# Kernel tuning notes

Hardware: AMD Instinct MI355X
Metric: run time of the kernel (lower is better)

Reference implementation:

```python
import jax, jax.numpy as jnp
import numpy as np
from jax import lax

L = 15      # time_conv_size
STRIDE = 2


def setup_inputs() -> dict:
    key = jax.random.key(0)
    k1, k2, k3 = jax.random.split(key, 3)
    x = jax.random.normal(k1, (8, 4096, 64), dtype=jnp.float32)
    w1 = jax.random.normal(k2, (L,), dtype=jnp.float32)
    w2 = jax.random.normal(k3, (L,), dtype=jnp.float32)
    return {"x": x, "w1": w1, "w2": w2}


def reference(x, w1, w2):
    # x: [B, T, C]; w1, w2: [L]
    B, T, C = x.shape
    p = L // 2
    # --- weighted local mean: mu[b,t,c] = sum_k w1[k] * x_pad[b,t+k,c] ---
    x_pad = jnp.pad(x, ((0, 0), (p, p), (0, 0)))
    mu = sum(w1[k] * x_pad[:, k:k + T, :] for k in range(L))  # [B,T,C]
    # --- centered diagonal bilinear (covariance) pooling ---
    xc_pad = jnp.pad(x - mu, ((0, 0), (p, p), (0, 0)))  # [B, T+2p, C]
    # strided window indices: I = ceil(T/STRIDE) windows of length L
    starts = jnp.arange(0, T, STRIDE)                   # [I]
    idx = starts[:, None] + jnp.arange(L)[None, :]      # [I, L]
    win = xc_pad[:, idx, :]                             # [B, I, L, C]
    sigma = jnp.einsum('bilc,l,bild->bicd', win, w2, win)
    I = starts.shape[0]
    sigma = sigma.reshape(B, I, C * C)
    mu_s = mu[:, ::STRIDE, :]                           # [B, I, C]
    out = jnp.concatenate([mu_s, sigma], axis=-1)       # [B, I, C + C*C]
    # K.l2_normalize over last axis (epsilon=1e-12)
    denom = lax.rsqrt(jnp.maximum(jnp.sum(out * out, axis=-1, keepdims=True), 1e-12))
    return out * denom
```

## Files before the change

kernel.cpp:

```cpp
#include <hip/hip_runtime.h>

#define Tdim 4096
#define Bdim 8
#define Cdim 64
#define Ldim 15
#define Idim 2048
#define OUTW 4160
#define G    4
#define RX   (2*G + 27)
#define RXC  (2*G + 13)

typedef float v4f __attribute__((ext_vector_type(4)));

__global__ __launch_bounds__(256, 6) void cbp_kernel(const float* __restrict__ x,
                                                     const float* __restrict__ w1,
                                                     const float* __restrict__ w2,
                                                     float* __restrict__ out) {
    __shared__ float xbuf[RX][64];
    __shared__ float xcs[RXC][64];
    __shared__ float mus[G][64];
    __shared__ float red[G][4];

    const int tid = threadIdx.x;
    const int blk = blockIdx.x;
    const int b  = blk >> 9;
    const int i0 = (blk & 511) << 2;
    const int s0 = i0 << 1;

    const float* xb = x + (size_t)b * (Tdim * Cdim);
    for (int v = tid; v < RX * 16; v += 256) {
        const int r  = v >> 4;
        const int c4 = (v & 15) << 2;
        const int t  = s0 - 14 + r;
        float4 val = make_float4(0.f, 0.f, 0.f, 0.f);
        if (t >= 0 && t < Tdim) val = *(const float4*)(xb + (size_t)t * Cdim + c4);
        *(float4*)(&xbuf[r][c4]) = val;
    }
    __syncthreads();

    for (int v = tid; v < RXC * 16; v += 256) {
        const int j  = v >> 4;
        const int c4 = (v & 15) << 2;
        const int t  = s0 - 7 + j;
        float4 m = make_float4(0.f, 0.f, 0.f, 0.f);
#pragma unroll
        for (int k = 0; k < Ldim; ++k) {
            const float w = w1[k];
            const float4 xv = *(const float4*)(&xbuf[j + k][c4]);
            m.x = fmaf(w, xv.x, m.x);
            m.y = fmaf(w, xv.y, m.y);
            m.z = fmaf(w, xv.z, m.z);
            m.w = fmaf(w, xv.w, m.w);
        }
        const float4 xv = *(const float4*)(&xbuf[j + 7][c4]);
        float4 xc = make_float4(0.f, 0.f, 0.f, 0.f);
        if (t >= 0 && t < Tdim)
            xc = make_float4(xv.x - m.x, xv.y - m.y, xv.z - m.z, xv.w - m.w);
        *(float4*)(&xcs[j][c4]) = xc;
        if (j >= 7 && j <= 13 && ((j - 7) & 1) == 0)
            *(float4*)(&mus[(j - 7) >> 1][c4]) = m;
    }
    __syncthreads();

    const int c0 = (tid >> 4) << 2;
    const int d0 = (tid & 15) << 2;

#pragma unroll
    for (int g = 0; g < G; ++g) {
        float acc[4][4];
#pragma unroll
        for (int cc = 0; cc < 4; ++cc)
#pragma unroll
            for (int dd = 0; dd < 4; ++dd) acc[cc][dd] = 0.f;

#pragma unroll
        for (int l = 0; l < Ldim; ++l) {
            const int r = 2 * g + l;
            const float4 xd = *(const float4*)(&xcs[r][d0]);
            const float4 xc = *(const float4*)(&xcs[r][c0]);
            const float w  = w2[l];
            const float a0 = w * xc.x, a1 = w * xc.y, a2 = w * xc.z, a3 = w * xc.w;
            acc[0][0] = fmaf(a0, xd.x, acc[0][0]);
            acc[0][1] = fmaf(a0, xd.y, acc[0][1]);
            acc[0][2] = fmaf(a0, xd.z, acc[0][2]);
            acc[0][3] = fmaf(a0, xd.w, acc[0][3]);
            acc[1][0] = fmaf(a1, xd.x, acc[1][0]);
            acc[1][1] = fmaf(a1, xd.y, acc[1][1]);
            acc[1][2] = fmaf(a1, xd.z, acc[1][2]);
            acc[1][3] = fmaf(a1, xd.w, acc[1][3]);
            acc[2][0] = fmaf(a2, xd.x, acc[2][0]);
            acc[2][1] = fmaf(a2, xd.y, acc[2][1]);
            acc[2][2] = fmaf(a2, xd.z, acc[2][2]);
            acc[2][3] = fmaf(a2, xd.w, acc[2][3]);
            acc[3][0] = fmaf(a3, xd.x, acc[3][0]);
            acc[3][1] = fmaf(a3, xd.y, acc[3][1]);
            acc[3][2] = fmaf(a3, xd.z, acc[3][2]);
            acc[3][3] = fmaf(a3, xd.w, acc[3][3]);
        }

        float ss = 0.f;
#pragma unroll
        for (int cc = 0; cc < 4; ++cc)
#pragma unroll
            for (int dd = 0; dd < 4; ++dd) ss = fmaf(acc[cc][dd], acc[cc][dd], ss);
        if (tid < Cdim) {
            const float m = mus[g][tid];
            ss = fmaf(m, m, ss);
        }
#pragma unroll
        for (int off = 32; off; off >>= 1) ss += __shfl_down(ss, off, 64);
        if ((tid & 63) == 0) red[g][tid >> 6] = ss;
        __syncthreads();

        const float sstot = red[g][0] + red[g][1] + red[g][2] + red[g][3];
        const float sc = rsqrtf(fmaxf(sstot, 1e-12f));

        float* orow = out + (size_t)(b * Idim + i0 + g) * OUTW;
        if (tid < 16) {
            const float4 m4 = *(const float4*)(&mus[g][tid << 2]);
            v4f mv = { m4.x * sc, m4.y * sc, m4.z * sc, m4.w * sc };
            __builtin_nontemporal_store(mv, (v4f*)(orow + (tid << 2)));
        }
        float* osig = orow + Cdim;
#pragma unroll
        for (int cc = 0; cc < 4; ++cc) {
            v4f v = { acc[cc][0] * sc, acc[cc][1] * sc,
                      acc[cc][2] * sc, acc[cc][3] * sc };
            __builtin_nontemporal_store(v, (v4f*)(osig + (c0 + cc) * Cdim + d0));
        }
    }
}

extern "C" void kernel_launch(void* const* d_in, const int* in_sizes, int n_in,
                              void* d_out, int out_size, void* d_ws, size_t ws_size,
                              hipStream_t stream) {
    const float* x  = (const float*)d_in[0];
    const float* w1 = (const float*)d_in[1];
    const float* w2 = (const float*)d_in[2];
    float* out = (float*)d_out;
    cbp_kernel<<<dim3(Bdim * (Idim / G)), dim3(256), 0, stream>>>(x, w1, w2, out);
}
```

Measured before the change: 332.4 us.

## Assign one window per wave with 8x8 register tiles and drop block sync

Each wave now computes one full 64x64 covariance window, with each lane accumulating an 8x8 tile. This lets the L2-norm reduction finish inside the wave with xor shuffles, so no block barrier is needed. Blocks handle 8 windows instead of 4, which halves the halo recompute per window, and launch bounds drop occupancy to 4. Output stores change from nontemporal to regular, which may affect write-streaming behavior.

```diff
diff --git a/kernel.cpp b/kernel.cpp
--- a/kernel.cpp
+++ b/kernel.cpp
@@ -6,25 +6,23 @@
 #define Ldim 15
 #define Idim 2048
 #define OUTW 4160
-#define G    4
-#define RX   (2*G + 27)
-#define RXC  (2*G + 13)
+#define NW   8
+#define RX   (2*NW + 27)
+#define RXC  (2*NW + 13)
+#define NBLK (Idim / NW)
 
-typedef float v4f __attribute__((ext_vector_type(4)));
-
-__global__ __launch_bounds__(256, 6) void cbp_kernel(const float* __restrict__ x,
+__global__ __launch_bounds__(256, 4) void cbp_kernel(const float* __restrict__ x,
                                                      const float* __restrict__ w1,
                                                      const float* __restrict__ w2,
                                                      float* __restrict__ out) {
     __shared__ float xbuf[RX][64];
     __shared__ float xcs[RXC][64];
-    __shared__ float mus[G][64];
-    __shared__ float red[G][4];
+    __shared__ float mus[NW][64];
 
     const int tid = threadIdx.x;
     const int blk = blockIdx.x;
-    const int b  = blk >> 9;
-    const int i0 = (blk & 511) << 2;
+    const int b  = blk >> 8;
+    const int i0 = (blk & (NBLK - 1)) * NW;
     const int s0 = i0 << 1;
 
     const float* xb = x + (size_t)b * (Tdim * Cdim);
@@ -57,76 +55,70 @@
         if (t >= 0 && t < Tdim)
             xc = make_float4(xv.x - m.x, xv.y - m.y, xv.z - m.z, xv.w - m.w);
         *(float4*)(&xcs[j][c4]) = xc;
-        if (j >= 7 && j <= 13 && ((j - 7) & 1) == 0)
+        if (j >= 7 && j <= 21 && (j & 1))
             *(float4*)(&mus[(j - 7) >> 1][c4]) = m;
     }
     __syncthreads();
 
-    const int c0 = (tid >> 4) << 2;
-    const int d0 = (tid & 15) << 2;
+    const int wid  = tid >> 6;
+    const int lane = tid & 63;
+    const int c0 = (lane >> 3) << 3;
+    const int d0 = (lane & 7) << 3;
 
 #pragma unroll
-    for (int g = 0; g < G; ++g) {
-        float acc[4][4];
+    for (int wi = 0; wi < NW / 4; ++wi) {
+        const int g = wid + (wi << 2);
+        float acc[8][8];
 #pragma unroll
-        for (int cc = 0; cc < 4; ++cc)
+        for (int i = 0; i < 8; ++i)
 #pragma unroll
-            for (int dd = 0; dd < 4; ++dd) acc[cc][dd] = 0.f;
+            for (int j = 0; j < 8; ++j) acc[i][j] = 0.f;
 
 #pragma unroll
         for (int l = 0; l < Ldim; ++l) {
             const int r = 2 * g + l;
-            const float4 xd = *(const float4*)(&xcs[r][d0]);
-            const float4 xc = *(const float4*)(&xcs[r][c0]);
-            const float w  = w2[l];
-            const float a0 = w * xc.x, a1 = w * xc.y, a2 = w * xc.z, a3 = w * xc.w;
-            acc[0][0] = fmaf(a0, xd.x, acc[0][0]);
-            acc[0][1] = fmaf(a0, xd.y, acc[0][1]);
-            acc[0][2] = fmaf(a0, xd.z, acc[0][2]);
-            acc[0][3] = fmaf(a0, xd.w, acc[0][3]);
-            acc[1][0] = fmaf(a1, xd.x, acc[1][0]);
-            acc[1][1] = fmaf(a1, xd.y, acc[1][1]);
-            acc[1][2] = fmaf(a1, xd.z, acc[1][2]);
-            acc[1][3] = fmaf(a1, xd.w, acc[1][3]);
-            acc[2][0] = fmaf(a2, xd.x, acc[2][0]);
-            acc[2][1] = fmaf(a2, xd.y, acc[2][1]);
-            acc[2][2] = fmaf(a2, xd.z, acc[2][2]);
-            acc[2][3] = fmaf(a2, xd.w, acc[2][3]);
-            acc[3][0] = fmaf(a3, xd.x, acc[3][0]);
-            acc[3][1] = fmaf(a3, xd.y, acc[3][1]);
-            acc[3][2] = fmaf(a3, xd.z, acc[3][2]);
-            acc[3][3] = fmaf(a3, xd.w, acc[3][3]);
+            const float4 xcA = *(const float4*)(&xcs[r][c0]);
+            const float4 xcB = *(const float4*)(&xcs[r][c0 + 4]);
+            const float4 xdA = *(const float4*)(&xcs[r][d0]);
+            const float4 xdB = *(const float4*)(&xcs[r][d0 + 4]);
+            const float w = w2[l];
+            float av[8], dv[8];
+            av[0] = w * xcA.x; av[1] = w * xcA.y; av[2] = w * xcA.z; av[3] = w * xcA.w;
+            av[4] = w * xcB.x; av[5] = w * xcB.y; av[6] = w * xcB.z; av[7] = w * xcB.w;
+            dv[0] = xdA.x; dv[1] = xdA.y; dv[2] = xdA.z; dv[3] = xdA.w;
+            dv[4] = xdB.x; dv[5] = xdB.y; dv[6] = xdB.z; dv[7] = xdB.w;
+#pragma unroll
+            for (int i = 0; i < 8; ++i)
+#pragma unroll
+                for (int j = 0; j < 8; ++j) acc[i][j] = fmaf(av[i], dv[j], acc[i][j]);
         }
 
         float ss = 0.f;
 #pragma unroll
-        for (int cc = 0; cc < 4; ++cc)
+        for (int i = 0; i < 8; ++i)
 #pragma unroll
-            for (int dd = 0; dd < 4; ++dd) ss = fmaf(acc[cc][dd], acc[cc][dd], ss);
-        if (tid < Cdim) {
-            const float m = mus[g][tid];
-            ss = fmaf(m, m, ss);
-        }
+            for (int j = 0; j < 8; ++j) ss = fmaf(acc[i][j], acc[i][j], ss);
+        const float mv = mus[g][lane];
+        ss = fmaf(mv, mv, ss);
 #pragma unroll
-        for (int off = 32; off; off >>= 1) ss += __shfl_down(ss, off, 64);
-        if ((tid & 63) == 0) red[g][tid >> 6] = ss;
-        __syncthreads();
-
-        const float sstot = red[g][0] + red[g][1] + red[g][2] + red[g][3];
-        const float sc = rsqrtf(fmaxf(sstot, 1e-12f));
+        for (int off = 32; off; off >>= 1) ss += __shfl_xor(ss, off, 64);
+        const float sc = rsqrtf(fmaxf(ss, 1e-12f));
 
         float* orow = out + (size_t)(b * Idim + i0 + g) * OUTW;
-        if (tid < 16) {
-            const float4 m4 = *(const float4*)(&mus[g][tid << 2]);
-            v4f mv = { m4.x * sc, m4.y * sc, m4.z * sc, m4.w * sc };
-            __builtin_nontemporal_store(mv, (v4f*)(orow + (tid << 2)));
+        if (lane < 16) {
+            float4 m4 = *(const float4*)(&mus[g][lane << 2]);
+            m4.x *= sc; m4.y *= sc; m4.z *= sc; m4.w *= sc;
+            *(float4*)(orow + (lane << 2)) = m4;
         }
         float* osig = orow + Cdim;
 #pragma unroll
-        for (int cc = 0; cc < 4; ++cc) {
-            v4f v = { acc[cc][0] * sc, acc[cc][1] * sc,
-                      acc[cc][2] * sc, acc[cc][3] * sc };
-            __builtin_nontemporal_store(v, (v4f*)(osig + (c0 + cc) * Cdim + d0));
+        for (int i = 0; i < 8; ++i) {
+            const float4 v0 = make_float4(acc[i][0] * sc, acc[i][1] * sc,
+                                          acc[i][2] * sc, acc[i][3] * sc);
+            const float4 v1 = make_float4(acc[i][4] * sc, acc[i][5] * sc,
+                                          acc[i][6] * sc, acc[i][7] * sc);
+            *(float4*)(osig + (c0 + i) * Cdim + d0)     = v0;
+            *(float4*)(osig + (c0 + i) * Cdim + d0 + 4) = v1;
         }
     }
 }
@@ -138,5 +130,5 @@
     const float* w1 = (const float*)d_in[1];
     const float* w2 = (const float*)d_in[2];
     float* out = (float*)d_out;
-    cbp_kernel<<<dim3(Bdim * (Idim / G)), dim3(256), 0, stream>>>(x, w1, w2, out);
+    cbp_kernel<<<dim3(Bdim * NBLK), dim3(256), 0, stream>>>(x, w1, w2, out);
 }
```

Measured after the change: 323.7 us. -2.6%, faster.
